# Performance work log

Measured on AMD Instinct MI355X. Metric: run time of the kernel, lower is better.

The kernel has to match this reference:

```python
import jax, jax.numpy as jnp
import numpy as np


def setup_inputs() -> dict:
    key = jax.random.key(0)
    k1, k2 = jax.random.split(key)
    B, S, D = 64, 2048, 1024
    hidden = jax.random.normal(k1, (B, S, D), dtype=jnp.float32)
    mask = jax.random.randint(k2, (B, S), 0, 2, dtype=jnp.int32)
    return {"hidden": hidden, "mask": mask}


def reference(hidden, mask):
    # hidden: [B, S, D], mask: [B, S] (0/1)
    m = mask.astype(hidden.dtype)
    cnt = jnp.sum(m, axis=1, keepdims=True)                 # [B, 1]
    masked_sum = jnp.einsum('bsd,bs->bd', hidden, m)        # [B, D]
    masked_mean = masked_sum / jnp.clip(cnt, 1.0)           # clamp(min=1.0)
    full_mean = jnp.mean(hidden, axis=1)                    # fallback when row has no valid tokens
    return jnp.where(cnt > 0, masked_mean, full_mean)
```

## Files before the change

### kernel.cpp

```cpp
#include <hip/hip_runtime.h>

#define BB 64
#define SS 2048
#define DD 1024
#define SCHUNK 64
#define NC (SS / SCHUNK)

typedef float f32x4 __attribute__((ext_vector_type(4)));

__global__ __launch_bounds__(256) void ep_partial(
    const float* __restrict__ hidden, const int* __restrict__ mask,
    float* __restrict__ wsm, float* __restrict__ wscnt)
{
    const int b    = blockIdx.x;
    const int c    = blockIdx.y;
    const int t    = threadIdx.x;
    const int lane = t & 63;

    __shared__ unsigned char sidx[SCHUNK];
    __shared__ int s_n;

    if (t < 64) {
        const int m = (mask[b * SS + c * SCHUNK + t] != 0) ? 1 : 0;
        const unsigned long long bal = __ballot(m);
        const int pre = __popcll(bal & ((1ull << lane) - 1ull));
        if (m) sidx[pre] = (unsigned char)t;
        if (t == 0) s_n = __popcll(bal);
    }
    __syncthreads();
    const int n1 = s_n;

    const unsigned rowoff = (unsigned)sidx[lane] * 4096u;

    const char* base = (const char*)hidden
                     + (size_t)(b * SS + c * SCHUNK) * DD * sizeof(float);
    const unsigned toff = (unsigned)t * 16u;

#define ROW(J)  (base + (unsigned)__builtin_amdgcn_readlane((int)rowoff, i + (J)) + toff)

    f32x4 am = {0.f, 0.f, 0.f, 0.f};

    int i = 0;
    for (; i + 16 <= n1; i += 16) {
        f32x4 v0  = *(const f32x4*)ROW(0);
        f32x4 v1  = *(const f32x4*)ROW(1);
        f32x4 v2  = *(const f32x4*)ROW(2);
        f32x4 v3  = *(const f32x4*)ROW(3);
        f32x4 v4  = *(const f32x4*)ROW(4);
        f32x4 v5  = *(const f32x4*)ROW(5);
        f32x4 v6  = *(const f32x4*)ROW(6);
        f32x4 v7  = *(const f32x4*)ROW(7);
        f32x4 v8  = *(const f32x4*)ROW(8);
        f32x4 v9  = *(const f32x4*)ROW(9);
        f32x4 v10 = *(const f32x4*)ROW(10);
        f32x4 v11 = *(const f32x4*)ROW(11);
        f32x4 v12 = *(const f32x4*)ROW(12);
        f32x4 v13 = *(const f32x4*)ROW(13);
        f32x4 v14 = *(const f32x4*)ROW(14);
        f32x4 v15 = *(const f32x4*)ROW(15);
        am += v0;  am += v1;  am += v2;  am += v3;
        am += v4;  am += v5;  am += v6;  am += v7;
        am += v8;  am += v9;  am += v10; am += v11;
        am += v12; am += v13; am += v14; am += v15;
    }
    for (; i + 4 <= n1; i += 4) {
        f32x4 v0 = *(const f32x4*)ROW(0);
        f32x4 v1 = *(const f32x4*)ROW(1);
        f32x4 v2 = *(const f32x4*)ROW(2);
        f32x4 v3 = *(const f32x4*)ROW(3);
        am += v0; am += v1; am += v2; am += v3;
    }
    for (; i < n1; ++i)
        am += *(const f32x4*)ROW(0);
#undef ROW

    reinterpret_cast<f32x4*>(wsm)[(size_t)(b * NC + c) * (DD / 4) + t] = am;
    if (t == 0) wscnt[b * NC + c] = (float)n1;
}

__global__ __launch_bounds__(64) void ep_finalize(
    const float* __restrict__ wsm, const float* __restrict__ wscnt,
    const float* __restrict__ hidden, float* __restrict__ out)
{
    const int b    = blockIdx.x;
    const int q    = blockIdx.y;
    const int lane = threadIdx.x;
    const int d4   = q * 64 + lane;

    float cnt = 0.f;
    #pragma unroll
    for (int c = 0; c < NC; ++c) cnt += wscnt[b * NC + c];

    const f32x4* pm = reinterpret_cast<const f32x4*>(wsm)
                      + (size_t)b * NC * (DD / 4) + d4;
    f32x4 am = {0.f, 0.f, 0.f, 0.f};
    #pragma unroll
    for (int c = 0; c < NC; ++c) am += pm[(size_t)c * (DD / 4)];

    f32x4 r;
    if (cnt > 0.f) {
        r.x = am.x / cnt; r.y = am.y / cnt; r.z = am.z / cnt; r.w = am.w / cnt;
    } else {
        const f32x4* hp = reinterpret_cast<const f32x4*>(hidden)
                          + (size_t)b * SS * (DD / 4) + d4;
        f32x4 af = {0.f, 0.f, 0.f, 0.f};
        for (int s = 0; s < SS; ++s) af += hp[(size_t)s * (DD / 4)];
        const float invS = 1.0f / (float)SS;
        r.x = af.x * invS; r.y = af.y * invS; r.z = af.z * invS; r.w = af.w * invS;
    }
    reinterpret_cast<f32x4*>(out)[(size_t)b * (DD / 4) + d4] = r;
}

extern "C" void kernel_launch(void* const* d_in, const int* in_sizes, int n_in,
                              void* d_out, int out_size, void* d_ws, size_t ws_size,
                              hipStream_t stream) {
    const float* hidden = (const float*)d_in[0];
    const int*   mask   = (const int*)d_in[1];
    float*       out    = (float*)d_out;

    float* wsm   = (float*)d_ws;
    float* wscnt = wsm + (size_t)BB * NC * DD;

    ep_partial<<<dim3(BB, NC), 256, 0, stream>>>(hidden, mask, wsm, wscnt);
    ep_finalize<<<dim3(BB, 4), 64, 0, stream>>>(wsm, wscnt, hidden, out);
}
```

Measured before the change: 633.6 us.

## Enlarge per-block sequence chunk with block-wide mask compaction and nontemporal loads

Each partial block now covers 256 sequence rows instead of 64. All four waves take part in the mask ballot, and per-wave counts are combined through shared memory into a block-wide compacted index list. Row indices are read from LDS instead of being broadcast with readlane, and hidden loads use nontemporal hints. The aim is to cut the number of partial sums the finalize kernel has to reduce and to avoid polluting the cache with streamed data. The cost is 4x fewer blocks, which can lower memory-level parallelism and occupancy on a large GPU, plus an extra barrier.

```diff
diff --git a/kernel.cpp b/kernel.cpp
--- a/kernel.cpp
+++ b/kernel.cpp
@@ -3,8 +3,8 @@
 #define BB 64
 #define SS 2048
 #define DD 1024
-#define SCHUNK 64
-#define NC (SS / SCHUNK)
+#define QC 8
+#define RCH (SS / QC)
 
 typedef float f32x4 __attribute__((ext_vector_type(4)));
 
@@ -13,69 +13,62 @@
     float* __restrict__ wsm, float* __restrict__ wscnt)
 {
     const int b    = blockIdx.x;
-    const int c    = blockIdx.y;
+    const int q    = blockIdx.y;
+    const int s0   = q * RCH;
     const int t    = threadIdx.x;
+    const int w    = t >> 6;
     const int lane = t & 63;
 
-    __shared__ unsigned char sidx[SCHUNK];
-    __shared__ int s_n;
+    __shared__ unsigned char sidx[RCH];
+    __shared__ int s_wcnt[4];
 
-    if (t < 64) {
-        const int m = (mask[b * SS + c * SCHUNK + t] != 0) ? 1 : 0;
-        const unsigned long long bal = __ballot(m);
-        const int pre = __popcll(bal & ((1ull << lane) - 1ull));
-        if (m) sidx[pre] = (unsigned char)t;
-        if (t == 0) s_n = __popcll(bal);
-    }
+    const int m = (mask[b * SS + s0 + t] != 0) ? 1 : 0;
+    const unsigned long long bal = __ballot(m);
+    const int pre = __popcll(bal & ((1ull << lane) - 1ull));
+    if (lane == 0) s_wcnt[w] = __popcll(bal);
     __syncthreads();
-    const int n1 = s_n;
-
-    const unsigned rowoff = (unsigned)sidx[lane] * 4096u;
+    int cbase = 0;
+    #pragma unroll
+    for (int j = 0; j < 4; ++j) cbase += (j < w) ? s_wcnt[j] : 0;
+    const int n1 = s_wcnt[0] + s_wcnt[1] + s_wcnt[2] + s_wcnt[3];
+    if (m) sidx[cbase + pre] = (unsigned char)t;
+    __syncthreads();
 
     const char* base = (const char*)hidden
-                     + (size_t)(b * SS + c * SCHUNK) * DD * sizeof(float);
+                     + (size_t)(b * SS + s0) * DD * sizeof(float);
     const unsigned toff = (unsigned)t * 16u;
 
-#define ROW(J)  (base + (unsigned)__builtin_amdgcn_readlane((int)rowoff, i + (J)) + toff)
+#define LD(J) __builtin_nontemporal_load( \
+        (const f32x4*)(base + (unsigned)sidx[i + (J)] * 4096u + toff))
 
     f32x4 am = {0.f, 0.f, 0.f, 0.f};
 
     int i = 0;
     for (; i + 16 <= n1; i += 16) {
-        f32x4 v0  = *(const f32x4*)ROW(0);
-        f32x4 v1  = *(const f32x4*)ROW(1);
-        f32x4 v2  = *(const f32x4*)ROW(2);
-        f32x4 v3  = *(const f32x4*)ROW(3);
-        f32x4 v4  = *(const f32x4*)ROW(4);
-        f32x4 v5  = *(const f32x4*)ROW(5);
-        f32x4 v6  = *(const f32x4*)ROW(6);
-        f32x4 v7  = *(const f32x4*)ROW(7);
-        f32x4 v8  = *(const f32x4*)ROW(8);
-        f32x4 v9  = *(const f32x4*)ROW(9);
-        f32x4 v10 = *(const f32x4*)ROW(10);
-        f32x4 v11 = *(const f32x4*)ROW(11);
-        f32x4 v12 = *(const f32x4*)ROW(12);
-        f32x4 v13 = *(const f32x4*)ROW(13);
-        f32x4 v14 = *(const f32x4*)ROW(14);
-        f32x4 v15 = *(const f32x4*)ROW(15);
+        f32x4 v0  = LD(0);  f32x4 v1  = LD(1);
+        f32x4 v2  = LD(2);  f32x4 v3  = LD(3);
+        f32x4 v4  = LD(4);  f32x4 v5  = LD(5);
+        f32x4 v6  = LD(6);  f32x4 v7  = LD(7);
+        f32x4 v8  = LD(8);  f32x4 v9  = LD(9);
+        f32x4 v10 = LD(10); f32x4 v11 = LD(11);
+        f32x4 v12 = LD(12); f32x4 v13 = LD(13);
+        f32x4 v14 = LD(14); f32x4 v15 = LD(15);
         am += v0;  am += v1;  am += v2;  am += v3;
         am += v4;  am += v5;  am += v6;  am += v7;
         am += v8;  am += v9;  am += v10; am += v11;
         am += v12; am += v13; am += v14; am += v15;
     }
     for (; i + 4 <= n1; i += 4) {
-        f32x4 v0 = *(const f32x4*)ROW(0);
-        f32x4 v1 = *(const f32x4*)ROW(1);
-        f32x4 v2 = *(const f32x4*)ROW(2);
-        f32x4 v3 = *(const f32x4*)ROW(3);
+        f32x4 v0 = LD(0); f32x4 v1 = LD(1);
+        f32x4 v2 = LD(2); f32x4 v3 = LD(3);
         am += v0; am += v1; am += v2; am += v3;
     }
     for (; i < n1; ++i)
-        am += *(const f32x4*)ROW(0);
-#undef ROW
+        am += LD(0);
+#undef LD
 
-    reinterpret_cast<f32x4*>(wsm)[(size_t)(b * NC + c) * (DD / 4) + t] = am;
-    if (t == 0) wscnt[b * NC + c] = (float)n1;
+    reinterpret_cast<f32x4*>(wsm)[(size_t)(b * QC + q) * (DD / 4) + t] = am;
+    if (t == 0) wscnt[b * QC + q] = (float)n1;
 }
 
 __global__ __launch_bounds__(64) void ep_finalize(
@@ -83,19 +76,19 @@
     const float* __restrict__ hidden, float* __restrict__ out)
 {
     const int b    = blockIdx.x;
-    const int q    = blockIdx.y;
+    const int qd   = blockIdx.y;
     const int lane = threadIdx.x;
-    const int d4   = q * 64 + lane;
+    const int d4   = qd * 64 + lane;
 
     float cnt = 0.f;
     #pragma unroll
-    for (int c = 0; c < NC; ++c) cnt += wscnt[b * NC + c];
+    for (int c = 0; c < QC; ++c) cnt += wscnt[b * QC + c];
 
     const f32x4* pm = reinterpret_cast<const f32x4*>(wsm)
-                      + (size_t)b * NC * (DD / 4) + d4;
+                      + (size_t)b * QC * (DD / 4) + d4;
     f32x4 am = {0.f, 0.f, 0.f, 0.f};
     #pragma unroll
-    for (int c = 0; c < NC; ++c) am += pm[(size_t)c * (DD / 4)];
+    for (int c = 0; c < QC; ++c) am += pm[(size_t)c * (DD / 4)];
 
     f32x4 r;
     if (cnt > 0.f) {
@@ -119,8 +112,8 @@
     float*       out    = (float*)d_out;
 
     float* wsm   = (float*)d_ws;
-    float* wscnt = wsm + (size_t)BB * NC * DD;
+    float* wscnt = wsm + (size_t)BB * QC * DD;
 
-    ep_partial<<<dim3(BB, NC), 256, 0, stream>>>(hidden, mask, wsm, wscnt);
+    ep_partial<<<dim3(BB, QC), 256, 0, stream>>>(hidden, mask, wsm, wscnt);
     ep_finalize<<<dim3(BB, 4), 64, 0, stream>>>(wsm, wscnt, hidden, out);
 }
```

Measured after the change: 614.0 us. -3.1%, faster.
